# Kernel tuning notes

Hardware: AMD Instinct MI355X
Metric: run time of the kernel (lower is better)

## Reference

```python
import jax, jax.numpy as jnp
import numpy as np

B, N, D, H, DH = 4, 1024, 1024, 16, 64
INNER = H * DH  # 1024


def setup_inputs() -> dict:
    key = jax.random.key(0)
    k0, k1, k2, k3 = jax.random.split(key, 4)
    x = jax.random.normal(k0, (B, N, D), dtype=jnp.float32)
    # float 0/1 padding mask per token
    mask = jax.random.randint(k1, (B, N), 0, 2).astype(jnp.float32)
    w_qkv = jax.random.normal(k2, (D, 3 * INNER), dtype=jnp.float32) * (D ** -0.5)
    w_out = jax.random.normal(k3, (INNER, D), dtype=jnp.float32) * (INNER ** -0.5)
    b_out = jnp.zeros((D,), dtype=jnp.float32)
    return {"x": x, "mask": mask, "w_qkv": w_qkv, "w_out": w_out, "b_out": b_out}


def reference(x, mask, w_qkv, w_out, b_out):
    scale = DH ** -0.5
    qkv = x @ w_qkv  # [B,N,3*INNER]
    q, k, v = jnp.split(qkv, 3, axis=-1)
    resh = lambda t: t.reshape(B, N, H, DH).transpose(0, 2, 1, 3)  # b h n d
    q, k, v = resh(q), resh(k), resh(v)
    dots = jnp.einsum('bhnd,bhmd->bhnm', q, k) * scale  # [B,H,N,N]
    # attn_bias = 1 - m_i*m_j; blocked where isclose(attn_bias, 1) i.e. pair ~ 0
    pair = mask[:, None, :, None] * mask[:, None, None, :]  # [B,1,N,N]
    blocked = jnp.isclose(1.0 - pair, jnp.ones_like(pair))
    dots = jnp.where(blocked, -jnp.inf, dots)
    # fully-masked-row fixup: rows that are all -inf get dots=0, attn forced to 0
    valid = jnp.any(dots != -jnp.inf, axis=-1, keepdims=True)  # [B,H,N,1]
    dots = jnp.where(valid, dots, 0.0)
    attn = jax.nn.softmax(dots, axis=-1)
    attn = jnp.where(valid, attn, 0.0)
    out = jnp.einsum('bhnm,bhmd->bhnd', attn, v)
    out = out.transpose(0, 2, 1, 3).reshape(B, N, INNER)
    return out @ w_out + b_out
```

## Files before the change

### kernel.cpp

```cpp
#include <hip/hip_runtime.h>

#define INF __builtin_inff()

typedef __attribute__((ext_vector_type(8))) short bf16x8;
typedef __attribute__((ext_vector_type(4))) short s16x4;
typedef __attribute__((ext_vector_type(4))) float f32x4;
typedef __attribute__((ext_vector_type(8))) unsigned short u16x8;
typedef __attribute__((ext_vector_type(4))) unsigned short u16x4;

#define MFMA16(a, b, c) __builtin_amdgcn_mfma_f32_16x16x32_bf16(a, b, c, 0, 0, 0)

#define ASYNC16(g, l) __builtin_amdgcn_global_load_lds( \
    (const __attribute__((address_space(1))) unsigned int*)(const void*)(g), \
    (__attribute__((address_space(3))) unsigned int*)(void*)(l), 16, 0, 0)

__device__ __forceinline__ unsigned short f2bf(float f) {
  union { float f; unsigned u; } v; v.f = f;
  unsigned r = v.u + 0x7fffu + ((v.u >> 16) & 1u);
  return (unsigned short)(r >> 16);
}

__global__ __launch_bounds__(256) void k_prep(
    const float* __restrict__ x, const float* __restrict__ mask,
    const float* __restrict__ wqkv, const float* __restrict__ wout,
    unsigned short* __restrict__ xc, unsigned short* __restrict__ wqkvt,
    unsigned short* __restrict__ woutt, unsigned short* __restrict__ perm,
    int* __restrict__ nvb) {
  __shared__ union {
    float tile[32][33];
    struct { unsigned short lperm[1024]; int wtot[4]; } sc;
  } sh;
  const int lid = blockIdx.x;
  const int t = threadIdx.x, lane = t & 63, wid = t >> 6;

  if (lid >= 4 && lid < 4100) {
    int id = lid - 4;
    const float* src; unsigned short* dst; int C, bc, br;
    if (id < 3072) { src = wqkv; dst = wqkvt; C = 3072; bc = (id % 96) * 32; br = (id / 96) * 32; }
    else { id -= 3072; src = wout; dst = woutt; C = 1024; bc = (id & 31) * 32; br = (id >> 5) * 32; }
    const int tx = t & 31, ty = t >> 5;
#pragma unroll
    for (int i = 0; i < 32; i += 8)
      sh.tile[ty + i][tx] = src[(size_t)(br + ty + i) * C + bc + tx];
    __syncthreads();
#pragma unroll
    for (int i = 0; i < 32; i += 8)
      dst[(size_t)(bc + ty + i) * 1024 + br + tx] = f2bf(sh.tile[tx][ty + i]);
    return;
  }

  const int b = (lid < 4) ? lid : ((lid - 4100) >> 8);
  float4 mv = ((const float4*)(mask + b * 1024))[t];
  int v0 = mv.x != 0.f, v1 = mv.y != 0.f, v2 = mv.z != 0.f, v3 = mv.w != 0.f;
  int cnt = v0 + v1 + v2 + v3;
  int pre = cnt;
#pragma unroll
  for (int d = 1; d < 64; d <<= 1) { int n = __shfl_up(pre, d); if (lane >= d) pre += n; }
  if (lane == 63) sh.sc.wtot[wid] = pre;
  __syncthreads();
  int base = 0;
#pragma unroll
  for (int i = 0; i < 4; ++i) if (i < wid) base += sh.sc.wtot[i];
  const int nvt = sh.sc.wtot[0] + sh.sc.wtot[1] + sh.sc.wtot[2] + sh.sc.wtot[3];
  int ex = base + pre - cnt;
  int vv[4] = { v0, v1, v2, v3 };

  if (lid < 4) {
#pragma unroll
    for (int j = 0; j < 4; ++j) {
      int tok = t * 4 + j;
      if (vv[j]) { perm[b * 1024 + ex] = (unsigned short)tok; ++ex; }
      else         perm[b * 1024 + nvt + (tok - ex)] = (unsigned short)tok;
    }
    if (t == 0) nvb[b] = nvt;
    return;
  }

#pragma unroll
  for (int j = 0; j < 4; ++j) {
    int tok = t * 4 + j;
    if (vv[j]) { sh.sc.lperm[ex] = (unsigned short)tok; ++ex; }
  }
  __syncthreads();
  const int s0 = ((lid - 4100) & 255) * 4;
  const int ce = (nvt + 127) & ~127;
#pragma unroll
  for (int j = 0; j < 4; ++j) {
    int slot = s0 + j;
    if (slot >= ce) continue;
    u16x4 o;
    if (slot < nvt) {
      int tok = sh.sc.lperm[slot];
      float4 f = ((const float4*)(x + ((size_t)(b * 1024 + tok)) * 1024))[t];
      o[0] = f2bf(f.x); o[1] = f2bf(f.y); o[2] = f2bf(f.z); o[3] = f2bf(f.w);
    } else {
      o[0] = o[1] = o[2] = o[3] = 0;
    }
    ((u16x4*)(xc + ((size_t)(b * 1024 + slot)) * 1024))[t] = o;
  }
}

__global__ __launch_bounds__(256) void k_gemm_qkv(
    const unsigned short* __restrict__ A, const unsigned short* __restrict__ Bt,
    const int* __restrict__ nvb,
    unsigned short* __restrict__ qcmp, unsigned short* __restrict__ kcmp,
    unsigned short* __restrict__ vt) {
  __shared__ unsigned short SH[32768];
  const int lid = blockIdx.x;
  const int xcd = lid & 7, i6 = lid >> 3;
  const int colt = xcd * 3 + (i6 % 3);
  const int rowt = i6 / 3;
  const int b = rowt >> 3, mt = rowt & 7;
  const int nv = nvb[b];
  if (mt * 128 >= nv) return;
  const int bm0 = mt * 128;
  const int bn0 = colt * 128;
  const size_t abase = ((size_t)(b * 1024 + bm0)) * 1024;
  const int t = threadIdx.x;
  const int lane = t & 63, wave = t >> 6;
  const int wm = (wave >> 1) * 64, wn = (wave & 1) * 64;
  const int lr = lane & 15, quad = lane >> 4;
  const int sw = lr & 7;
  f32x4 acc[4][4] = {};
  auto stage = [&](int pp, int k0) {
    unsigned short* As = SH + pp * 16384;
    unsigned short* Bs = As + 8192;
#pragma unroll
    for (int j = 0; j < 4; ++j) {
      int idx = t + j * 256;
      int row = idx >> 3;
      int g = (idx ^ row) & 7;
      ASYNC16(&A[abase + (size_t)row * 1024 + k0 + g * 8], &As[idx * 8]);
      ASYNC16(&Bt[((size_t)(bn0 + row)) * 1024 + k0 + g * 8], &Bs[idx * 8]);
    }
  };
  stage(0, 0);
  for (int it = 0; it < 16; ++it) {
    const int pp = it & 1;
    __syncthreads();
    if (it + 1 < 16) stage(1 - pp, (it + 1) * 64);
    const unsigned short* As = SH + pp * 16384;
    const unsigned short* Bs = As + 8192;
#pragma unroll
    for (int ks = 0; ks < 2; ++ks) {
      bf16x8 af[4], bfr[4];
#pragma unroll
      for (int i = 0; i < 4; ++i)
        af[i] = *(const bf16x8*)(&As[(wm + i * 16 + lr) * 64 + (((ks * 4 + quad) ^ sw)) * 8]);
#pragma unroll
      for (int j = 0; j < 4; ++j)
        bfr[j] = *(const bf16x8*)(&Bs[(wn + j * 16 + lr) * 64 + (((ks * 4 + quad) ^ sw)) * 8]);
#pragma unroll
      for (int i = 0; i < 4; ++i)
#pragma unroll
        for (int j = 0; j < 4; ++j)
          acc[i][j] = MFMA16(af[i], bfr[j], acc[i][j]);
    }
  }
  const int sec = bn0 >> 10;
  const int js0 = bn0 & 1023;
#pragma unroll
  for (int hh = 0; hh < 2; ++hh) {
    __syncthreads();
    if ((wave >> 1) == hh) {
#pragma unroll
      for (int i = 0; i < 4; ++i)
#pragma unroll
        for (int j = 0; j < 4; ++j)
#pragma unroll
          for (int r = 0; r < 4; ++r)
            SH[(i * 16 + quad * 4 + r) * 136 + wn + j * 16 + lr] = f2bf(acc[i][j][r]);
    }
    __syncthreads();
    if (sec < 2) {
      unsigned short* dstT = sec ? kcmp : qcmp;
#pragma unroll
      for (int rr = 0; rr < 4; ++rr) {
        int lrow = (t >> 4) + rr * 16;
        int ck = t & 15;
        int slot = bm0 + hh * 64 + lrow;
        int js = js0 + ck * 8;
        int h = js >> 6, d = js & 63;
        u16x8 v = *(u16x8*)(&SH[lrow * 136 + ck * 8]);
        *(u16x8*)(&dstT[(((size_t)(b * 16 + h)) * 1024 + slot) * 64 + d]) = v;
      }
    } else {
      const int c = t & 127, seg = t >> 7;
      const int js = js0 + c, h = js >> 6, d = js & 63;
      unsigned short* vrow =
          &vt[(((size_t)(b * 16 + h)) * 64 + d) * 1024 + bm0 + hh * 64 + seg * 32];
#pragma unroll
      for (int s4 = 0; s4 < 4; ++s4) {
        u16x8 v;
#pragma unroll
        for (int s = 0; s < 8; ++s) v[s] = SH[(seg * 32 + s4 * 8 + s) * 136 + c];
        *(u16x8*)(vrow + s4 * 8) = v;
      }
    }
  }
}

__global__ __launch_bounds__(256, 3) void k_attn(
    const unsigned short* __restrict__ qcmp, const unsigned short* __restrict__ kcmp,
    const unsigned short* __restrict__ vtc, const int* __restrict__ nvb,
    unsigned short* __restrict__ aoc) {
  __shared__ unsigned short Ks[2][4096];
  __shared__ unsigned short Vs[2][4096];
  __shared__ unsigned short P[4][16 * 72];
  const int bx = blockIdx.x;
  const int bh = (bx & 7) + 8 * (bx >> 7);
  const int qcb = (bx >> 3) & 15;
  const int b = bh >> 4;
  const int nv = nvb[b];
  if (qcb * 64 >= nv) return;
  const int t = threadIdx.x;
  const int wave = t >> 6, lane = t & 63;
  const int lr = lane & 15, quad = lane >> 4;
  const int q0 = qcb * 64 + wave * 16;
  const unsigned short* qp = qcmp + ((size_t)bh << 16);
  const unsigned short* kp = kcmp + ((size_t)bh << 16);
  const unsigned short* vp = vtc + ((size_t)bh << 16);
  unsigned short* Pw = P[wave];
  bf16x8 qv0 = *(const bf16x8*)(qp + (q0 + lr) * 64 + quad * 8);
  bf16x8 qv1 = *(const bf16x8*)(qp + (q0 + lr) * 64 + 32 + quad * 8);
  float m = -INF, l = 0.f;
  f32x4 o[4] = {};
  const int sw = lr & 7;
  const int nk = (nv + 63) >> 6;
  auto stage = [&](int pp, int kc0) {
#pragma unroll
    for (int ld = 0; ld < 2; ++ld) {
      int idx = t + ld * 256;
      int row = idx >> 3;
      int g = (idx ^ row) & 7;
      ASYNC16(kp + (kc0 + row) * 64 + g * 8, &Ks[pp][idx * 8]);
      ASYNC16(vp + (size_t)row * 1024 + kc0 + g * 8, &Vs[pp][idx * 8]);
    }
  };
  stage(0, 0);
  for (int it = 0; it < nk; ++it) {
    const int pp = it & 1;
    const int kc0 = it * 64;
    __syncthreads();
    if (it + 1 < nk) stage(1 - pp, kc0 + 64);
    f32x4 st[4];
#pragma unroll
    for (int tt = 0; tt < 4; ++tt) {
      int krow = tt * 16 + lr;
      bf16x8 k0 = *(const bf16x8*)(&Ks[pp][krow * 64 + ((quad ^ sw)) * 8]);
      bf16x8 k1 = *(const bf16x8*)(&Ks[pp][krow * 64 + (((4 + quad) ^ sw)) * 8]);
      f32x4 c = {};
      c = MFMA16(k0, qv0, c);
      c = MFMA16(k1, qv1, c);
      st[tt] = c;
    }
    float tm = -INF;
#pragma unroll
    for (int tt = 0; tt < 4; ++tt) {
#pragma unroll
      for (int r = 0; r < 4; ++r) {
        int slot = kc0 + tt * 16 + quad * 4 + r;
        float v = (slot < nv) ? st[tt][r] * 0.125f : -INF;
        st[tt][r] = v;
        tm = fmaxf(tm, v);
      }
    }
    tm = fmaxf(tm, __shfl_xor(tm, 16));
    tm = fmaxf(tm, __shfl_xor(tm, 32));
    float mn = fmaxf(m, tm);
    float alpha = __expf(m - mn);
    if (m == -INF) alpha = 1.f;
    float ps = 0.f;
#pragma unroll
    for (int tt = 0; tt < 4; ++tt) {
      s16x4 pv;
#pragma unroll
      for (int r = 0; r < 4; ++r) {
        float pe = __expf(st[tt][r] - mn);
        ps += pe;
        pv[r] = (short)f2bf(pe);
      }
      *(s16x4*)(&Pw[lr * 72 + tt * 16 + quad * 4]) = pv;
    }
    ps += __shfl_xor(ps, 16);
    ps += __shfl_xor(ps, 32);
    l = l * alpha + ps;
    m = mn;
    float ar[4];
#pragma unroll
    for (int r = 0; r < 4; ++r) ar[r] = __shfl(alpha, quad * 4 + r);
#pragma unroll
    for (int jj = 0; jj < 4; ++jj)
#pragma unroll
      for (int r = 0; r < 4; ++r) o[jj][r] *= ar[r];
#pragma unroll
    for (int sh = 0; sh < 2; ++sh) {
      bf16x8 pa = *(const bf16x8*)(&Pw[lr * 72 + sh * 32 + quad * 8]);
#pragma unroll
      for (int jj = 0; jj < 4; ++jj) {
        bf16x8 vbf = *(const bf16x8*)(&Vs[pp][(jj * 16 + lr) * 64 + (((sh * 4 + quad) ^ sw)) * 8]);
        o[jj] = MFMA16(pa, vbf, o[jj]);
      }
    }
  }
  float inv = 1.f / l;
  float ir[4];
#pragma unroll
  for (int r = 0; r < 4; ++r) ir[r] = __shfl(inv, quad * 4 + r);
  const int h = bh & 15;
#pragma unroll
  for (int r = 0; r < 4; ++r) {
    int slot = q0 + quad * 4 + r;
    if (slot < nv) {
      size_t rowb = ((size_t)(b * 1024 + slot)) * 1024 + h * 64;
#pragma unroll
      for (int jj = 0; jj < 4; ++jj)
        aoc[rowb + jj * 16 + lr] = f2bf(o[jj][r] * ir[r]);
    }
  }
}

__global__ __launch_bounds__(256) void k_gemm_fin(
    const unsigned short* __restrict__ A, const unsigned short* __restrict__ Bt,
    const unsigned short* __restrict__ perm, const int* __restrict__ nvb,
    const float* __restrict__ bias, float* __restrict__ C) {
  __shared__ unsigned short SH[24576];
  const int lid = blockIdx.x;
  const int t = threadIdx.x;
  if (lid >= 512) {
    const int idx = lid - 512;
    const int b = idx >> 6, ch = idx & 63;
    const int nv = nvb[b];
    const float4 bv = ((const float4*)bias)[t];
    for (int s = nv + ch * 8; s < 1024; s += 512) {
#pragma unroll
      for (int j = 0; j < 8; ++j) {
        int slot = s + j;
        if (slot < 1024) {
          int tok = perm[b * 1024 + slot];
          ((float4*)(C + ((size_t)(b * 1024 + tok)) * 1024))[t] = bv;
        }
      }
    }
    return;
  }
  const int col = lid & 7;
  const int rt = lid >> 3;
  const int b = rt >> 4, mt = rt & 15;
  const int nv = nvb[b];
  if (mt * 64 >= nv) return;
  const int bm0 = mt * 64;
  const int bn0 = col * 128;
  const size_t abase = ((size_t)(b * 1024 + bm0)) * 1024;
  const int lane = t & 63, wave = t >> 6;
  const int wm = (wave >> 1) * 32, wn = (wave & 1) * 64;
  const int lr = lane & 15, quad = lane >> 4;
  const int sw = lr & 7;
  f32x4 acc[2][4] = {};
  auto stage = [&](int pp, int k0) {
    unsigned short* As = SH + pp * 12288;
    unsigned short* Bs = As + 4096;
#pragma unroll
    for (int j = 0; j < 2; ++j) {
      int idx = t + j * 256;
      int row = idx >> 3;
      int g = (idx ^ row) & 7;
      ASYNC16(&A[abase + (size_t)row * 1024 + k0 + g * 8], &As[idx * 8]);
    }
#pragma unroll
    for (int j = 0; j < 4; ++j) {
      int idx = t + j * 256;
      int row = idx >> 3;
      int g = (idx ^ row) & 7;
      ASYNC16(&Bt[((size_t)(bn0 + row)) * 1024 + k0 + g * 8], &Bs[idx * 8]);
    }
  };
  stage(0, 0);
  for (int it = 0; it < 16; ++it) {
    const int pp = it & 1;
    __syncthreads();
    if (it + 1 < 16) stage(1 - pp, (it + 1) * 64);
    const unsigned short* As = SH + pp * 12288;
    const unsigned short* Bs = As + 4096;
#pragma unroll
    for (int ks = 0; ks < 2; ++ks) {
      bf16x8 af[2], bfr[4];
#pragma unroll
      for (int i = 0; i < 2; ++i)
        af[i] = *(const bf16x8*)(&As[(wm + i * 16 + lr) * 64 + (((ks * 4 + quad) ^ sw)) * 8]);
#pragma unroll
      for (int j = 0; j < 4; ++j)
        bfr[j] = *(const bf16x8*)(&Bs[(wn + j * 16 + lr) * 64 + (((ks * 4 + quad) ^ sw)) * 8]);
#pragma unroll
      for (int i = 0; i < 2; ++i)
#pragma unroll
        for (int j = 0; j < 4; ++j)
          acc[i][j] = MFMA16(af[i], bfr[j], acc[i][j]);
    }
  }
#pragma unroll
  for (int i = 0; i < 2; ++i)
#pragma unroll
    for (int r = 0; r < 4; ++r) {
      int slot = bm0 + wm + i * 16 + quad * 4 + r;
      if (slot < nv) {
        int tok = perm[b * 1024 + slot];
        size_t rowb = ((size_t)(b * 1024 + tok)) * 1024;
#pragma unroll
        for (int j = 0; j < 4; ++j) {
          int c = bn0 + wn + j * 16 + lr;
          C[rowb + c] = acc[i][j][r] + bias[c];
        }
      }
    }
}

extern "C" void kernel_launch(void* const* d_in, const int* in_sizes, int n_in,
                              void* d_out, int out_size, void* d_ws, size_t ws_size,
                              hipStream_t stream) {
  const float* x    = (const float*)d_in[0];
  const float* mask = (const float*)d_in[1];
  const float* wqkv = (const float*)d_in[2];
  const float* wout = (const float*)d_in[3];
  const float* bout = (const float*)d_in[4];
  float* out = (float*)d_out;
  char* ws = (char*)d_ws;
  unsigned short* xc    = (unsigned short*)(ws);
  unsigned short* aoc   = (unsigned short*)(ws);
  unsigned short* wqkvt = (unsigned short*)(ws + (size_t)( 8 << 20));
  unsigned short* woutt = (unsigned short*)(ws + (size_t)(14 << 20));
  unsigned short* qcmp  = (unsigned short*)(ws + (size_t)(16 << 20));
  unsigned short* kcmp  = (unsigned short*)(ws + (size_t)(24 << 20));
  unsigned short* vt    = (unsigned short*)(ws + (size_t)(32 << 20));
  unsigned short* perm  = (unsigned short*)(ws + (size_t)(40 << 20));
  int*            nvb   = (int*)           (ws + (size_t)(40 << 20) + 8192);

  k_prep<<<5124, 256, 0, stream>>>(x, mask, wqkv, wout, xc, wqkvt, woutt, perm, nvb);
  k_gemm_qkv<<<768, 256, 0, stream>>>(xc, wqkvt, nvb, qcmp, kcmp, vt);
  k_attn<<<1024, 256, 0, stream>>>(qcmp, kcmp, vt, nvb, aoc);
  k_gemm_fin<<<768, 256, 0, stream>>>(aoc, woutt, perm, nvb, bout, out);
}
```

Baseline: 146.9 us.

## Fold softmax scale into Q, lazy rescale, exp2, vectorized epilogues, move bias fill

Q is pre-scaled by scale*log2(e) in the QKV GEMM epilogue so attention can use exp2 with no per-element multiply. The online softmax now rescales the accumulator only when the running max grows by more than a threshold, and skips masking on full key tiles. MFMA sections are bracketed with s_setprio. Both the attention output and the final GEMM output are staged through LDS so global stores are vectorized. The fill of masked output rows with bias moves from the final GEMM into extra blocks of the prep kernel, indexed directly by mask. The lazy-rescale threshold risks overflow in the bf16 probabilities if the bound is loose.

```diff
diff --git a/kernel.cpp b/kernel.cpp
--- a/kernel.cpp
+++ b/kernel.cpp
@@ -14,6 +14,14 @@
     (const __attribute__((address_space(1))) unsigned int*)(const void*)(g), \
     (__attribute__((address_space(3))) unsigned int*)(void*)(l), 16, 0, 0)
 
+#if __has_builtin(__builtin_amdgcn_exp2f)
+#define EXP2(x) __builtin_amdgcn_exp2f(x)
+#else
+#define EXP2(x) exp2f(x)
+#endif
+
+#define QSCALE 0.18033688011112042f
+
 __device__ __forceinline__ unsigned short f2bf(float f) {
   union { float f; unsigned u; } v; v.f = f;
   unsigned r = v.u + 0x7fffu + ((v.u >> 16) & 1u);
@@ -25,7 +33,7 @@
     const float* __restrict__ wqkv, const float* __restrict__ wout,
     unsigned short* __restrict__ xc, unsigned short* __restrict__ wqkvt,
     unsigned short* __restrict__ woutt, unsigned short* __restrict__ perm,
-    int* __restrict__ nvb) {
+    int* __restrict__ nvb, const float* __restrict__ bias, float* __restrict__ C) {
   __shared__ union {
     float tile[32][33];
     struct { unsigned short lperm[1024]; int wtot[4]; } sc;
@@ -33,15 +41,28 @@
   const int lid = blockIdx.x;
   const int t = threadIdx.x, lane = t & 63, wid = t >> 6;
 
+  if (lid >= 5124) {
+    const int idx = lid - 5124;
+    const int b = idx >> 6, g = idx & 63;
+    const float4 bv = ((const float4*)bias)[t];
+    const float* mrow = mask + b * 1024 + g * 16;
+#pragma unroll
+    for (int j = 0; j < 16; ++j) {
+      if (mrow[j] == 0.f)
+        ((float4*)(C + ((size_t)(b * 1024 + g * 16 + j)) * 1024))[t] = bv;
+    }
+    return;
+  }
+
   if (lid >= 4 && lid < 4100) {
     int id = lid - 4;
-    const float* src; unsigned short* dst; int C, bc, br;
-    if (id < 3072) { src = wqkv; dst = wqkvt; C = 3072; bc = (id % 96) * 32; br = (id / 96) * 32; }
-    else { id -= 3072; src = wout; dst = woutt; C = 1024; bc = (id & 31) * 32; br = (id >> 5) * 32; }
+    const float* src; unsigned short* dst; int Cc, bc, br;
+    if (id < 3072) { src = wqkv; dst = wqkvt; Cc = 3072; bc = (id % 96) * 32; br = (id / 96) * 32; }
+    else { id -= 3072; src = wout; dst = woutt; Cc = 1024; bc = (id & 31) * 32; br = (id >> 5) * 32; }
     const int tx = t & 31, ty = t >> 5;
 #pragma unroll
     for (int i = 0; i < 32; i += 8)
-      sh.tile[ty + i][tx] = src[(size_t)(br + ty + i) * C + bc + tx];
+      sh.tile[ty + i][tx] = src[(size_t)(br + ty + i) * Cc + bc + tx];
     __syncthreads();
 #pragma unroll
     for (int i = 0; i < 32; i += 8)
@@ -159,6 +180,7 @@
   }
   const int sec = bn0 >> 10;
   const int js0 = bn0 & 1023;
+  const float qs = (sec == 0) ? QSCALE : 1.f;
 #pragma unroll
   for (int hh = 0; hh < 2; ++hh) {
     __syncthreads();
@@ -169,7 +191,7 @@
         for (int j = 0; j < 4; ++j)
 #pragma unroll
           for (int r = 0; r < 4; ++r)
-            SH[(i * 16 + quad * 4 + r) * 136 + wn + j * 16 + lr] = f2bf(acc[i][j][r]);
+            SH[(i * 16 + quad * 4 + r) * 136 + wn + j * 16 + lr] = f2bf(acc[i][j][r] * qs);
     }
     __syncthreads();
     if (sec < 2) {
@@ -244,6 +266,7 @@
     __syncthreads();
     if (it + 1 < nk) stage(1 - pp, kc0 + 64);
     f32x4 st[4];
+    __builtin_amdgcn_s_setprio(1);
 #pragma unroll
     for (int tt = 0; tt < 4; ++tt) {
       int krow = tt * 16 + lr;
@@ -254,29 +277,36 @@
       c = MFMA16(k1, qv1, c);
       st[tt] = c;
     }
+    __builtin_amdgcn_s_setprio(0);
     float tm = -INF;
-#pragma unroll
-    for (int tt = 0; tt < 4; ++tt) {
-#pragma unroll
-      for (int r = 0; r < 4; ++r) {
-        int slot = kc0 + tt * 16 + quad * 4 + r;
-        float v = (slot < nv) ? st[tt][r] * 0.125f : -INF;
-        st[tt][r] = v;
-        tm = fmaxf(tm, v);
-      }
+    if (kc0 + 64 <= nv) {
+#pragma unroll
+      for (int tt = 0; tt < 4; ++tt)
+#pragma unroll
+        for (int r = 0; r < 4; ++r) tm = fmaxf(tm, st[tt][r]);
+    } else {
+#pragma unroll
+      for (int tt = 0; tt < 4; ++tt)
+#pragma unroll
+        for (int r = 0; r < 4; ++r) {
+          int slot = kc0 + tt * 16 + quad * 4 + r;
+          float v = (slot < nv) ? st[tt][r] : -INF;
+          st[tt][r] = v;
+          tm = fmaxf(tm, v);
+        }
     }
     tm = fmaxf(tm, __shfl_xor(tm, 16));
     tm = fmaxf(tm, __shfl_xor(tm, 32));
     float mn = fmaxf(m, tm);
-    float alpha = __expf(m - mn);
-    if (m == -INF) alpha = 1.f;
+    const bool resc = !__all(tm <= m + 8.f);
+    if (!resc) mn = m;
     float ps = 0.f;
 #pragma unroll
     for (int tt = 0; tt < 4; ++tt) {
       s16x4 pv;
 #pragma unroll
       for (int r = 0; r < 4; ++r) {
-        float pe = __expf(st[tt][r] - mn);
+        float pe = EXP2(st[tt][r] - mn);
         ps += pe;
         pv[r] = (short)f2bf(pe);
       }
@@ -284,15 +314,21 @@
     }
     ps += __shfl_xor(ps, 16);
     ps += __shfl_xor(ps, 32);
-    l = l * alpha + ps;
-    m = mn;
-    float ar[4];
-#pragma unroll
-    for (int r = 0; r < 4; ++r) ar[r] = __shfl(alpha, quad * 4 + r);
-#pragma unroll
-    for (int jj = 0; jj < 4; ++jj)
-#pragma unroll
-      for (int r = 0; r < 4; ++r) o[jj][r] *= ar[r];
+    if (resc) {
+      float alpha = EXP2(m - mn);
+      l = l * alpha + ps;
+      m = mn;
+      float ar[4];
+#pragma unroll
+      for (int r = 0; r < 4; ++r) ar[r] = __shfl(alpha, quad * 4 + r);
+#pragma unroll
+      for (int jj = 0; jj < 4; ++jj)
+#pragma unroll
+        for (int r = 0; r < 4; ++r) o[jj][r] *= ar[r];
+    } else {
+      l += ps;
+    }
+    __builtin_amdgcn_s_setprio(1);
 #pragma unroll
     for (int sh = 0; sh < 2; ++sh) {
       bf16x8 pa = *(const bf16x8*)(&Pw[lr * 72 + sh * 32 + quad * 8]);
@@ -302,20 +338,25 @@
         o[jj] = MFMA16(pa, vbf, o[jj]);
       }
     }
+    __builtin_amdgcn_s_setprio(0);
   }
   float inv = 1.f / l;
   float ir[4];
 #pragma unroll
   for (int r = 0; r < 4; ++r) ir[r] = __shfl(inv, quad * 4 + r);
+#pragma unroll
+  for (int jj = 0; jj < 4; ++jj)
+#pragma unroll
+    for (int r = 0; r < 4; ++r)
+      Pw[(quad * 4 + r) * 72 + jj * 16 + lr] = f2bf(o[jj][r] * ir[r]);
   const int h = bh & 15;
-#pragma unroll
-  for (int r = 0; r < 4; ++r) {
-    int slot = q0 + quad * 4 + r;
-    if (slot < nv) {
-      size_t rowb = ((size_t)(b * 1024 + slot)) * 1024 + h * 64;
-#pragma unroll
-      for (int jj = 0; jj < 4; ++jj)
-        aoc[rowb + jj * 16 + lr] = f2bf(o[jj][r] * ir[r]);
+  const int slot = q0 + lr;
+  if (slot < nv) {
+    size_t rowb = ((size_t)(b * 1024 + slot)) * 1024 + h * 64;
+#pragma unroll
+    for (int p = 0; p < 2; ++p) {
+      u16x8 v8 = *(const u16x8*)(&Pw[lr * 72 + (quad + p * 4) * 8]);
+      *(u16x8*)(&aoc[rowb + (quad + p * 4) * 8]) = v8;
     }
   }
 }
@@ -327,23 +368,6 @@
   __shared__ unsigned short SH[24576];
   const int lid = blockIdx.x;
   const int t = threadIdx.x;
-  if (lid >= 512) {
-    const int idx = lid - 512;
-    const int b = idx >> 6, ch = idx & 63;
-    const int nv = nvb[b];
-    const float4 bv = ((const float4*)bias)[t];
-    for (int s = nv + ch * 8; s < 1024; s += 512) {
-#pragma unroll
-      for (int j = 0; j < 8; ++j) {
-        int slot = s + j;
-        if (slot < 1024) {
-          int tok = perm[b * 1024 + slot];
-          ((float4*)(C + ((size_t)(b * 1024 + tok)) * 1024))[t] = bv;
-        }
-      }
-    }
-    return;
-  }
   const int col = lid & 7;
   const int rt = lid >> 3;
   const int b = rt >> 4, mt = rt & 15;
@@ -398,21 +422,29 @@
           acc[i][j] = MFMA16(af[i], bfr[j], acc[i][j]);
     }
   }
+  __syncthreads();
+  float* W = (float*)SH + wave * 2176;
+  float bj[4];
+#pragma unroll
+  for (int j = 0; j < 4; ++j) bj[j] = bias[bn0 + wn + j * 16 + lr];
 #pragma unroll
   for (int i = 0; i < 2; ++i)
 #pragma unroll
-    for (int r = 0; r < 4; ++r) {
-      int slot = bm0 + wm + i * 16 + quad * 4 + r;
-      if (slot < nv) {
-        int tok = perm[b * 1024 + slot];
-        size_t rowb = ((size_t)(b * 1024 + tok)) * 1024;
-#pragma unroll
-        for (int j = 0; j < 4; ++j) {
-          int c = bn0 + wn + j * 16 + lr;
-          C[rowb + c] = acc[i][j][r] + bias[c];
-        }
-      }
-    }
+    for (int j = 0; j < 4; ++j)
+#pragma unroll
+      for (int r = 0; r < 4; ++r)
+        W[(i * 16 + quad * 4 + r) * 68 + j * 16 + lr] = acc[i][j][r] + bj[j];
+#pragma unroll
+  for (int p = 0; p < 8; ++p) {
+    int fi = p * 64 + lane;
+    int row = fi >> 4, c4 = fi & 15;
+    int slot = bm0 + wm + row;
+    if (slot < nv) {
+      int tok = perm[b * 1024 + slot];
+      float4 v4 = *(const float4*)(&W[row * 68 + c4 * 4]);
+      *(float4*)(&C[((size_t)(b * 1024 + tok)) * 1024 + bn0 + wn + c4 * 4]) = v4;
+    }
+  }
 }
 
 extern "C" void kernel_launch(void* const* d_in, const int* in_sizes, int n_in,
@@ -435,8 +467,8 @@
   unsigned short* perm  = (unsigned short*)(ws + (size_t)(40 << 20));
   int*            nvb   = (int*)           (ws + (size_t)(40 << 20) + 8192);
 
-  k_prep<<<5124, 256, 0, stream>>>(x, mask, wqkv, wout, xc, wqkvt, woutt, perm, nvb);
+  k_prep<<<5380, 256, 0, stream>>>(x, mask, wqkv, wout, xc, wqkvt, woutt, perm, nvb, bout, out);
   k_gemm_qkv<<<768, 256, 0, stream>>>(xc, wqkvt, nvb, qcmp, kcmp, vt);
   k_attn<<<1024, 256, 0, stream>>>(qcmp, kcmp, vt, nvb, aoc);
-  k_gemm_fin<<<768, 256, 0, stream>>>(aoc, woutt, perm, nvb, bout, out);
-}
+  k_gemm_fin<<<512, 256, 0, stream>>>(aoc, woutt, perm, nvb, bout, out);
+}
```

Measured after the change: 142.9 us. -2.7%, faster.
